# Optimization experiments

Measured on AMD Instinct MI355X. Metric: run time of the kernel, lower is better.

The kernel has to match this reference:

```python
import jax, jax.numpy as jnp
import numpy as np

B, T, D, DS, EXP = 1, 2048, 512, 32, 2
EPS = 1e-6


def setup_inputs() -> dict:
    key = jax.random.key(0)
    ks = jax.random.split(key, 16)
    g = lambda k, shape, s: jax.random.normal(k, shape, jnp.float32) * s
    x = jax.random.normal(ks[0], (B, T, D), jnp.float32)
    inv = D ** -0.5
    return {
        "x": x,
        "norm_w": jnp.ones((D,), jnp.float32),
        "W_in": g(ks[1], (D, 2 * D), inv),
        "conv_w": g(ks[2], (D, 1, 4), 0.5),          # depthwise, torch layout (O, I/groups, K)
        "conv_b": g(ks[3], (D,), 0.1),
        "W_dt": g(ks[4], (D, D), 0.01 * inv),
        "b_dt": jnp.full((D,), -8.0, jnp.float32) + g(ks[5], (D,), 0.1),  # Mamba-style small-dt init
        "W_B": g(ks[6], (D, DS), inv),
        "W_C": g(ks[7], (D, DS), inv),
        "W_out": g(ks[8], (D, D), inv),
        "log_A": jnp.log(jnp.linspace(1.0, 16.0, D)).astype(jnp.float32),
        "D_param": jnp.ones((D,), jnp.float32),
        "W_ffn1": g(ks[9], (D, EXP * D), inv),
        "W_ffn2": g(ks[10], (EXP * D, D), (EXP * D) ** -0.5),
        "W_merge": g(ks[11], (2 * D, D), (2 * D) ** -0.5),
    }


def _ssm_scan(xs, dt, Bm, Cm, A):
    # cumsum-based parallel scan, exactly as ParallelSSMScan.forward
    log_a = jnp.clip(dt * A[None, None, :], -20.0, 20.0)      # [B,T,D]
    cum = jnp.cumsum(log_a, axis=1)                            # [B,T,D]
    dtx = dt * xs                                              # [B,T,D]
    inp = dtx[..., None] * Bm[:, :, None, :]                   # [B,T,D,ds]
    scaled = jnp.exp(-cum)[..., None] * inp                    # [B,T,D,ds]
    prefix = jnp.cumsum(scaled, axis=1)                        # [B,T,D,ds]
    h_all = jnp.exp(cum)[..., None] * prefix                   # [B,T,D,ds]
    return jnp.einsum('btds,bts->btd', h_all, Cm)


def _forward(x, norm_w, W_in, conv_w, conv_b, W_dt, b_dt, W_B, W_C, W_out,
             log_A, D_param, W_ffn1, W_ffn2, W_merge):
    r = x
    rms = jnp.sqrt(jnp.mean(x * x, axis=-1, keepdims=True) + EPS)
    xn = x / rms * norm_w
    xz = xn @ W_in
    xs, z = jnp.split(xz, 2, axis=-1)
    # causal depthwise conv (padding=3 then [:T] == left-pad 3, valid)
    xt = jnp.transpose(xs, (0, 2, 1))                          # [B,D,T]
    c = jax.lax.conv_general_dilated(
        xt, conv_w, window_strides=(1,), padding=[(3, 0)],
        feature_group_count=D, dimension_numbers=('NCH', 'OIH', 'NCH'))
    c = c + conv_b[None, :, None]
    xs = jax.nn.silu(jnp.transpose(c, (0, 2, 1)))              # [B,T,D]
    dt = jax.nn.softplus(xs @ W_dt + b_dt)
    Bm = xs @ W_B
    Cm = xs @ W_C
    A = -jnp.exp(log_A)
    y = _ssm_scan(xs, dt, Bm, Cm, A)
    y_ssm = (y + xs * D_param) * jax.nn.silu(z)
    y_ssm = y_ssm @ W_out
    y_ffn = jax.nn.gelu(xn @ W_ffn1, approximate=False) @ W_ffn2
    y = jnp.concatenate([y_ssm, y_ffn], axis=-1) @ W_merge
    # dropout in eval mode -> identity
    return r + y


def reference(x, norm_w, W_in, conv_w, conv_b, W_dt, b_dt, W_B, W_C, W_out,
              log_A, D_param, W_ffn1, W_ffn2, W_merge):
    return _forward(x, norm_w, W_in, conv_w, conv_b, W_dt, b_dt, W_B, W_C,
                    W_out, log_A, D_param, W_ffn1, W_ffn2, W_merge)
```

## Files before the change

kernel.cpp:

```cpp
#include <hip/hip_runtime.h>
#include <math.h>

#define T_LEN 2048
#define D_DIM 512
#define NCHUNK 64
#define CLEN 32

typedef __bf16 bf16x8 __attribute__((ext_vector_type(8)));
typedef float f32x4 __attribute__((ext_vector_type(4)));

typedef const __attribute__((address_space(1))) void gvoid;
typedef __attribute__((address_space(3))) void lvoid;

__device__ __forceinline__ void async16(const void* g, void* l) {
  __builtin_amdgcn_global_load_lds((gvoid*)g, (lvoid*)l, 16, 0, 0);
}

__device__ __forceinline__ float silu_f(float x) { return x / (1.f + __expf(-x)); }
__device__ __forceinline__ float softplus_f(float x) {
  return fmaxf(x, 0.f) + log1pf(__expf(-fabsf(x)));
}
__device__ __forceinline__ float gelu_f(float x) {
  return 0.5f * x * (1.f + erff(x * 0.70710678118654752440f));
}
__device__ __forceinline__ unsigned short f2bf(float f) {
  union { float f; unsigned u; } v; v.f = f;
  unsigned r = v.u + 0x7FFF + ((v.u >> 16) & 1);
  return (unsigned short)(r >> 16);
}

__global__ __launch_bounds__(256) void rmsnorm_kernel(
    const float* __restrict__ x, const float* __restrict__ w,
    unsigned short* __restrict__ xn) {
  const int t = blockIdx.x;
  const float2 v = reinterpret_cast<const float2*>(x + (size_t)t * D_DIM)[threadIdx.x];
  float ss = v.x * v.x + v.y * v.y;
#pragma unroll
  for (int m = 1; m < 64; m <<= 1) ss += __shfl_xor(ss, m);
  __shared__ float wsum[4];
  if ((threadIdx.x & 63) == 0) wsum[threadIdx.x >> 6] = ss;
  __syncthreads();
  const float tot = wsum[0] + wsum[1] + wsum[2] + wsum[3];
  const float scale = rsqrtf(tot * (1.f / D_DIM) + 1e-6f);
  const float2 wv = reinterpret_cast<const float2*>(w)[threadIdx.x];
  ushort2 o;
  o.x = f2bf(v.x * scale * wv.x);
  o.y = f2bf(v.y * scale * wv.y);
  reinterpret_cast<ushort2*>(xn + (size_t)t * D_DIM)[threadIdx.x] = o;
}

struct TransJobs {
  const float* src[8];
  unsigned short* dst[8];
  int K[8];
  int N[8];
  int tr[8];
  int b0[9];
};

__global__ __launch_bounds__(256) void prep_weights_kernel(TransJobs J) {
  __shared__ float tile[32][33];
  const int b = blockIdx.x;
  int ji = 0;
#pragma unroll
  for (int i = 1; i < 8; ++i) ji += (b >= J.b0[i]) ? 1 : 0;
  const float* __restrict__ src = J.src[ji];
  unsigned short* __restrict__ dst = J.dst[ji];
  const int K = J.K[ji], N = J.N[ji];
  const int rel = b - J.b0[ji];
  const int nbx = N >> 5;
  const int bx = rel % nbx, by = rel / nbx;
  const int k0 = by * 32, n0 = bx * 32;
  const int i = threadIdx.x & 31;
  const int r = threadIdx.x >> 5;
  if (J.tr[ji]) {
#pragma unroll
    for (int p = 0; p < 4; ++p) {
      const int kk = r + p * 8;
      tile[kk][i] = src[(size_t)(k0 + kk) * N + n0 + i];
    }
    __syncthreads();
#pragma unroll
    for (int p = 0; p < 4; ++p) {
      const int nn = r + p * 8;
      dst[(size_t)(n0 + nn) * K + k0 + i] = f2bf(tile[i][nn]);
    }
  } else {
#pragma unroll
    for (int p = 0; p < 4; ++p) {
      const int kk = r + p * 8;
      dst[(size_t)(k0 + kk) * N + n0 + i] = f2bf(src[(size_t)(k0 + kk) * N + n0 + i]);
    }
  }
}

__device__ __forceinline__ void gemm64_core(
    const unsigned short* __restrict__ Abf, const unsigned short* __restrict__ Btbf,
    int nt, int lda8, int ldb8, int brow, int bcol,
    bf16x8* __restrict__ As, bf16x8* __restrict__ Bs, f32x4 acc[2][2]) {
  const int tid = threadIdx.x;
  const int lane = tid & 63;
  const int w = tid >> 6;
  const int wrow = (w >> 1) * 32;
  const int wcol = (w & 1) * 32;
  const bf16x8* __restrict__ A8 = reinterpret_cast<const bf16x8*>(Abf);
  const bf16x8* __restrict__ B8 = reinterpret_cast<const bf16x8*>(Btbf);

  const int lr = lane >> 3;
  const int ls = (lane & 7) ^ lr;
  bf16x8* ldsA0 = &As[(w * 8) * 8];
  bf16x8* ldsA1 = &As[(32 + w * 8) * 8];
  bf16x8* ldsB0 = &Bs[(w * 8) * 8];
  bf16x8* ldsB1 = &Bs[(32 + w * 8) * 8];
  const size_t a0 = (size_t)(brow + w * 8 + lr) * lda8 + ls;
  const size_t a1 = (size_t)(brow + 32 + w * 8 + lr) * lda8 + ls;
  const size_t b0 = (size_t)(bcol + w * 8 + lr) * ldb8 + ls;
  const size_t b1 = (size_t)(bcol + 32 + w * 8 + lr) * ldb8 + ls;

  for (int t = 0; t < nt; ++t) {
    const int kb = t * 8;
    async16(A8 + a0 + kb, ldsA0);
    async16(A8 + a1 + kb, ldsA1);
    async16(B8 + b0 + kb, ldsB0);
    async16(B8 + b1 + kb, ldsB1);
    __syncthreads();
#pragma unroll
    for (int kk = 0; kk < 2; ++kk) {
      const int slot = kk * 4 + (lane >> 4);
      bf16x8 af[2], bf_[2];
#pragma unroll
      for (int m = 0; m < 2; ++m) {
        const int r = wrow + m * 16 + (lane & 15);
        af[m] = As[r * 8 + (slot ^ (r & 7))];
      }
#pragma unroll
      for (int n = 0; n < 2; ++n) {
        const int r = wcol + n * 16 + (lane & 15);
        bf_[n] = Bs[r * 8 + (slot ^ (r & 7))];
      }
#pragma unroll
      for (int m = 0; m < 2; ++m)
#pragma unroll
        for (int n = 0; n < 2; ++n)
          acc[m][n] = __builtin_amdgcn_mfma_f32_16x16x32_bf16(af[m], bf_[n], acc[m][n], 0, 0, 0);
    }
    __syncthreads();
  }
}

__global__ __launch_bounds__(256) void gemm64_in(
    const unsigned short* __restrict__ Abf, const unsigned short* __restrict__ Btbf,
    float* __restrict__ xz, unsigned short* __restrict__ comb) {
  __shared__ bf16x8 As[512];
  __shared__ bf16x8 Bs[512];
  f32x4 acc[2][2];
#pragma unroll
  for (int m = 0; m < 2; ++m)
#pragma unroll
    for (int n = 0; n < 2; ++n) acc[m][n] = {0.f, 0.f, 0.f, 0.f};
  const int brow = blockIdx.y * 64;
  const int bcol = blockIdx.x * 64;
  gemm64_core(Abf, Btbf, 8, 64, 64, brow, bcol, As, Bs, acc);

  const int lane = threadIdx.x & 63;
  const int w = threadIdx.x >> 6;
  const int wrow = (w >> 1) * 32;
  const int wcol = (w & 1) * 32;
#pragma unroll
  for (int m = 0; m < 2; ++m) {
#pragma unroll
    for (int n = 0; n < 2; ++n) {
      const int col = bcol + wcol + n * 16 + (lane & 15);
#pragma unroll
      for (int j = 0; j < 4; ++j) {
        const int row = brow + wrow + m * 16 + (lane >> 4) * 4 + j;
        const float v = acc[m][n][j];
        if (col < 1024) {
          xz[(size_t)row * 1024 + col] = v;
        } else {
          comb[(size_t)row * 1536 + 512 + (col - 1024)] = f2bf(gelu_f(v));
        }
      }
    }
  }
}

__global__ __launch_bounds__(256) void gemm64_dtbc(
    const unsigned short* __restrict__ Abf, const unsigned short* __restrict__ Btbf,
    float* __restrict__ dt, float* __restrict__ Bm, float* __restrict__ Cm,
    const float* __restrict__ bias) {
  __shared__ bf16x8 As[512];
  __shared__ bf16x8 Bs[512];
  f32x4 acc[2][2];
#pragma unroll
  for (int m = 0; m < 2; ++m)
#pragma unroll
    for (int n = 0; n < 2; ++n) acc[m][n] = {0.f, 0.f, 0.f, 0.f};
  const int brow = blockIdx.y * 64;
  const int bcol = blockIdx.x * 64;
  gemm64_core(Abf, Btbf, 8, 64, 64, brow, bcol, As, Bs, acc);

  const int lane = threadIdx.x & 63;
  const int w = threadIdx.x >> 6;
  const int wrow = (w >> 1) * 32;
  const int wcol = (w & 1) * 32;
#pragma unroll
  for (int m = 0; m < 2; ++m) {
#pragma unroll
    for (int n = 0; n < 2; ++n) {
      const int col = bcol + wcol + n * 16 + (lane & 15);
#pragma unroll
      for (int j = 0; j < 4; ++j) {
        const int row = brow + wrow + m * 16 + (lane >> 4) * 4 + j;
        const float v = acc[m][n][j];
        if (col < 512) {
          dt[(size_t)row * 512 + col] = softplus_f(v + bias[col]);
        } else {
          const int s = col - 512;
          float* p = (s < 32) ? Bm : Cm;
          p[(size_t)row * 32 + (s & 31)] = v;
        }
      }
    }
  }
}

__global__ __launch_bounds__(256) void combine_kernel(
    const unsigned short* __restrict__ WmT, const unsigned short* __restrict__ WoutBF,
    const unsigned short* __restrict__ Wf2BF, unsigned short* __restrict__ WcombT) {
  const int z = blockIdx.z;
  if (z == 0 && blockIdx.x >= 8) return;
  __shared__ bf16x8 As[512];
  __shared__ bf16x8 Bs[512];
  const unsigned short* A = z ? (WmT + 512) : WmT;
  const unsigned short* Bt = z ? Wf2BF : WoutBF;
  const int coff = z ? 512 : 0;
  f32x4 acc[2][2];
#pragma unroll
  for (int m = 0; m < 2; ++m)
#pragma unroll
    for (int n = 0; n < 2; ++n) acc[m][n] = {0.f, 0.f, 0.f, 0.f};
  const int brow = blockIdx.y * 64;
  const int bcol = blockIdx.x * 64;
  gemm64_core(A, Bt, 8, 128, 64, brow, bcol, As, Bs, acc);

  const int lane = threadIdx.x & 63;
  const int w = threadIdx.x >> 6;
  const int wrow = (w >> 1) * 32;
  const int wcol = (w & 1) * 32;
#pragma unroll
  for (int m = 0; m < 2; ++m) {
#pragma unroll
    for (int n = 0; n < 2; ++n) {
      const int col = bcol + wcol + n * 16 + (lane & 15);
#pragma unroll
      for (int j = 0; j < 4; ++j) {
        const int row = brow + wrow + m * 16 + (lane >> 4) * 4 + j;
        WcombT[(size_t)row * 1536 + coff + col] = f2bf(acc[m][n][j]);
      }
    }
  }
}

__global__ __launch_bounds__(256) void gemm64_merge(
    const unsigned short* __restrict__ Abf, const unsigned short* __restrict__ Btbf,
    float* __restrict__ out, const float* __restrict__ resid) {
  __shared__ bf16x8 As[512];
  __shared__ bf16x8 Bs[512];
  f32x4 acc[2][2];
#pragma unroll
  for (int m = 0; m < 2; ++m)
#pragma unroll
    for (int n = 0; n < 2; ++n) acc[m][n] = {0.f, 0.f, 0.f, 0.f};
  const int brow = blockIdx.y * 64;
  const int bcol = blockIdx.x * 64;
  gemm64_core(Abf, Btbf, 24, 192, 192, brow, bcol, As, Bs, acc);

  const int lane = threadIdx.x & 63;
  const int w = threadIdx.x >> 6;
  const int wrow = (w >> 1) * 32;
  const int wcol = (w & 1) * 32;
#pragma unroll
  for (int m = 0; m < 2; ++m) {
#pragma unroll
    for (int n = 0; n < 2; ++n) {
      const int col = bcol + wcol + n * 16 + (lane & 15);
#pragma unroll
      for (int j = 0; j < 4; ++j) {
        const int row = brow + wrow + m * 16 + (lane >> 4) * 4 + j;
        out[(size_t)row * 512 + col] = resid[(size_t)row * 512 + col] + acc[m][n][j];
      }
    }
  }
}

__global__ __launch_bounds__(256) void conv_silu_kernel(
    const float* __restrict__ xz, const float* __restrict__ cw,
    const float* __restrict__ cb, float* __restrict__ xs,
    unsigned short* __restrict__ xs_bf) {
  const int idx = blockIdx.x * 256 + threadIdx.x;
  const int t = idx >> 9;
  const int d = idx & 511;
  const float4 w = reinterpret_cast<const float4*>(cw)[d];
  float acc = cb[d];
  const float wk[4] = {w.x, w.y, w.z, w.w};
#pragma unroll
  for (int k = 0; k < 4; ++k) {
    const int tt = t - 3 + k;
    if (tt >= 0) acc = fmaf(xz[(size_t)tt * 1024 + d], wk[k], acc);
  }
  const float s = silu_f(acc);
  xs[idx] = s;
  xs_bf[idx] = f2bf(s);
}

__global__ __launch_bounds__(256) void prep_gram_kernel(
    const float* __restrict__ dt, const float* __restrict__ xs,
    const float* __restrict__ Bm, const float* __restrict__ Cm,
    const float* __restrict__ log_A,
    unsigned short* __restrict__ U_T, float* __restrict__ E,
    float* __restrict__ V, float* __restrict__ Pc,
    unsigned short* __restrict__ Gm) {
  __shared__ float4 Bls4[CLEN * 8];
  __shared__ float Bls[32][33], Cls[32][33];

  if (blockIdx.x < 128) {
    const int c = blockIdx.x >> 1;
    const int d = (blockIdx.x & 1) * 256 + threadIdx.x;
    Bls4[threadIdx.x] = reinterpret_cast<const float4*>(Bm + c * CLEN * 32)[threadIdx.x];
    __syncthreads();

    const float A = -__expf(log_A[d]);
    float cum = 0.f;
    float e = 1.f;
    float vacc[32];
#pragma unroll
    for (int s = 0; s < 32; ++s) vacc[s] = 0.f;
    unsigned pk[16];
#pragma unroll
    for (int t = 0; t < CLEN; ++t) {
      const int tg = c * CLEN + t;
      const float dtv = dt[(size_t)tg * D_DIM + d];
      const float xv  = xs[(size_t)tg * D_DIM + d];
      const float la = fminf(fmaxf(dtv * A, -20.f), 20.f);
      cum += la;
      e = __expf(cum);
      E[(size_t)tg * D_DIM + d] = e;
      const float u = __expf(-cum) * dtv * xv;
      const unsigned short ub = f2bf(u);
      if ((t & 1) == 0) pk[t >> 1] = (unsigned)ub;
      else              pk[t >> 1] |= ((unsigned)ub) << 16;
#pragma unroll
      for (int s4 = 0; s4 < 8; ++s4) {
        const float4 b = Bls4[t * 8 + s4];
        vacc[s4 * 4 + 0] = fmaf(u, b.x, vacc[s4 * 4 + 0]);
        vacc[s4 * 4 + 1] = fmaf(u, b.y, vacc[s4 * 4 + 1]);
        vacc[s4 * 4 + 2] = fmaf(u, b.z, vacc[s4 * 4 + 2]);
        vacc[s4 * 4 + 3] = fmaf(u, b.w, vacc[s4 * 4 + 3]);
      }
    }
    {
      uint4* dst = reinterpret_cast<uint4*>(U_T + (size_t)d * T_LEN + c * CLEN);
      dst[0] = make_uint4(pk[0], pk[1], pk[2], pk[3]);
      dst[1] = make_uint4(pk[4], pk[5], pk[6], pk[7]);
      dst[2] = make_uint4(pk[8], pk[9], pk[10], pk[11]);
      dst[3] = make_uint4(pk[12], pk[13], pk[14], pk[15]);
    }
    {
      float4* dst = reinterpret_cast<float4*>(V + ((size_t)c * D_DIM + d) * 32);
#pragma unroll
      for (int s4 = 0; s4 < 8; ++s4)
        dst[s4] = make_float4(vacc[s4 * 4], vacc[s4 * 4 + 1], vacc[s4 * 4 + 2], vacc[s4 * 4 + 3]);
    }
    Pc[c * D_DIM + d] = e;
  } else {
    const int c = blockIdx.x - 128;
    {
      const int t = threadIdx.x >> 3;
      const int s4 = threadIdx.x & 7;
      const float4 b = reinterpret_cast<const float4*>(Bm + (c * CLEN + t) * 32)[s4];
      const float4 cc = reinterpret_cast<const float4*>(Cm + (c * CLEN + t) * 32)[s4];
      Bls[t][s4 * 4 + 0] = b.x;  Bls[t][s4 * 4 + 1] = b.y;
      Bls[t][s4 * 4 + 2] = b.z;  Bls[t][s4 * 4 + 3] = b.w;
      Cls[t][s4 * 4 + 0] = cc.x; Cls[t][s4 * 4 + 1] = cc.y;
      Cls[t][s4 * 4 + 2] = cc.z; Cls[t][s4 * 4 + 3] = cc.w;
    }
    __syncthreads();
    const int t = threadIdx.x >> 3;
    const int tp0 = (threadIdx.x & 7) * 4;
    float g[4];
#pragma unroll
    for (int q = 0; q < 4; ++q) {
      const int tp = tp0 + q;
      float acc = 0.f;
      if (tp <= t) {
#pragma unroll
        for (int s = 0; s < 32; ++s) acc = fmaf(Cls[t][s], Bls[tp][s], acc);
      }
      g[q] = acc;
    }
    ushort4 o;
    o.x = f2bf(g[0]); o.y = f2bf(g[1]); o.z = f2bf(g[2]); o.w = f2bf(g[3]);
    reinterpret_cast<ushort4*>(Gm + c * 1024)[threadIdx.x] = o;
  }
}

__global__ __launch_bounds__(256) void state_scan_kernel(
    const float* __restrict__ V, const float* __restrict__ Pc,
    float* __restrict__ Hin) {
  const int gt = blockIdx.x * 256 + threadIdx.x;
  const int d = gt >> 5;
  float h = 0.f;
  for (int c = 0; c < NCHUNK; ++c) {
    Hin[c * 16384 + gt] = h;
    h = Pc[c * D_DIM + d] * (h + V[c * 16384 + gt]);
  }
}

__global__ __launch_bounds__(256) void ssm_out_kernel(
    const unsigned short* __restrict__ Gm, const unsigned short* __restrict__ U_T,
    const float* __restrict__ Hin, const float* __restrict__ Cm,
    const float* __restrict__ E, const float* __restrict__ xs,
    const float* __restrict__ Dp, const float* __restrict__ xz,
    unsigned short* __restrict__ comb) {
  const int c = blockIdx.x;
  const int dt0 = blockIdx.y * 64;
  __shared__ bf16x8 Als[32 * 8];
  __shared__ bf16x8 Bls[64 * 8];
  const int tid = threadIdx.x;

  if (tid < 128) {
    const int t = tid >> 2, q = tid & 3;
    Als[t * 8 + (q ^ (t & 7))] =
        *reinterpret_cast<const bf16x8*>(Gm + c * 1024 + t * 32 + q * 8);
  } else {
    const int i = tid - 128;
    const int t = i >> 2, q = i & 3;
    const float* cp = Cm + (c * CLEN + t) * 32 + q * 8;
    const float4 c0 = *reinterpret_cast<const float4*>(cp);
    const float4 c1 = *reinterpret_cast<const float4*>(cp + 4);
    union { bf16x8 v; unsigned short u[8]; } wv;
    wv.u[0] = f2bf(c0.x); wv.u[1] = f2bf(c0.y); wv.u[2] = f2bf(c0.z); wv.u[3] = f2bf(c0.w);
    wv.u[4] = f2bf(c1.x); wv.u[5] = f2bf(c1.y); wv.u[6] = f2bf(c1.z); wv.u[7] = f2bf(c1.w);
    Als[t * 8 + ((4 + q) ^ (t & 7))] = wv.v;
  }
  {
    const int dd = tid >> 2, q = tid & 3;
    Bls[dd * 8 + (q ^ (dd & 7))] = *reinterpret_cast<const bf16x8*>(
        U_T + (size_t)(dt0 + dd) * T_LEN + c * CLEN + q * 8);
    const float* hp = Hin + ((size_t)c * D_DIM + dt0 + dd) * 32 + q * 8;
    const float4 h0 = *reinterpret_cast<const float4*>(hp);
    const float4 h1 = *reinterpret_cast<const float4*>(hp + 4);
    union { bf16x8 v; unsigned short u[8]; } wv;
    wv.u[0] = f2bf(h0.x); wv.u[1] = f2bf(h0.y); wv.u[2] = f2bf(h0.z); wv.u[3] = f2bf(h0.w);
    wv.u[4] = f2bf(h1.x); wv.u[5] = f2bf(h1.y); wv.u[6] = f2bf(h1.z); wv.u[7] = f2bf(h1.w);
    Bls[dd * 8 + ((4 + q) ^ (dd & 7))] = wv.v;
  }
  __syncthreads();

  const int lane = tid & 63;
  const int w = tid >> 6;
  const int wcol = w * 16;
  f32x4 acc[2];
  acc[0] = {0.f, 0.f, 0.f, 0.f};
  acc[1] = {0.f, 0.f, 0.f, 0.f};
#pragma unroll
  for (int kk = 0; kk < 2; ++kk) {
    const int slot = kk * 4 + (lane >> 4);
    const int rb = wcol + (lane & 15);
    const bf16x8 bfrag = Bls[rb * 8 + (slot ^ (rb & 7))];
#pragma unroll
    for (int m = 0; m < 2; ++m) {
      const int r = m * 16 + (lane & 15);
      const bf16x8 afrag = Als[r * 8 + (slot ^ (r & 7))];
      acc[m] = __builtin_amdgcn_mfma_f32_16x16x32_bf16(afrag, bfrag, acc[m], 0, 0, 0);
    }
  }
  const int dg = dt0 + wcol + (lane & 15);
  const float dpv = Dp[dg];
#pragma unroll
  for (int m = 0; m < 2; ++m) {
#pragma unroll
    for (int j = 0; j < 4; ++j) {
      const int tg = c * CLEN + m * 16 + (lane >> 4) * 4 + j;
      const float y = E[(size_t)tg * D_DIM + dg] * acc[m][j];
      const float xv = xs[(size_t)tg * D_DIM + dg];
      const float zv = xz[(size_t)tg * 1024 + 512 + dg];
      comb[(size_t)tg * 1536 + dg] = f2bf(fmaf(xv, dpv, y) * silu_f(zv));
    }
  }
}

extern "C" void kernel_launch(void* const* d_in, const int* in_sizes, int n_in,
                              void* d_out, int out_size, void* d_ws, size_t ws_size,
                              hipStream_t stream) {
  const float* x      = (const float*)d_in[0];
  const float* norm_w = (const float*)d_in[1];
  const float* W_in   = (const float*)d_in[2];
  const float* conv_w = (const float*)d_in[3];
  const float* conv_b = (const float*)d_in[4];
  const float* W_dt   = (const float*)d_in[5];
  const float* b_dt   = (const float*)d_in[6];
  const float* W_B    = (const float*)d_in[7];
  const float* W_C    = (const float*)d_in[8];
  const float* W_out  = (const float*)d_in[9];
  const float* log_A  = (const float*)d_in[10];
  const float* D_par  = (const float*)d_in[11];
  const float* W_ffn1 = (const float*)d_in[12];
  const float* W_ffn2 = (const float*)d_in[13];
  const float* W_mrg  = (const float*)d_in[14];
  float* out = (float*)d_out;

  const size_t M1 = 1u << 20;
  char* ws = (char*)d_ws;
  size_t off = 0;
  auto alloc_f = [&](size_t n) { float* p = (float*)(ws + off); off += n * 4; return p; };
  auto alloc_h = [&](size_t n) { unsigned short* p = (unsigned short*)(ws + off); off += n * 2; return p; };

  float* xz  = alloc_f(2 * M1);
  float* xs  = alloc_f(M1);
  float* dt  = alloc_f(M1);
  float* E   = alloc_f(M1);
  float* V   = alloc_f(M1);
  float* Hin = alloc_f(M1);
  float* Bm  = alloc_f(1 << 16);
  float* Cm  = alloc_f(1 << 16);
  float* Pc  = alloc_f(NCHUNK * D_DIM);
  unsigned short* U_T    = alloc_h(M1);
  unsigned short* Gm     = alloc_h(NCHUNK * 1024);
  unsigned short* xn_bf  = alloc_h(M1);
  unsigned short* xs_bf  = alloc_h(M1);
  unsigned short* comb   = alloc_h(2048 * 1536);
  unsigned short* WinF1T = alloc_h(2048 * 512);
  unsigned short* WdtBCT = alloc_h(576 * 512);
  unsigned short* WmT    = alloc_h(512 * 1024);
  unsigned short* WoutBF = alloc_h(512 * 512);
  unsigned short* Wf2BF  = alloc_h(1024 * 512);
  unsigned short* WcombT = alloc_h(512 * 1536);

  TransJobs J;
  J.src[0] = W_in;   J.dst[0] = WinF1T;              J.K[0] = 512;  J.N[0] = 1024; J.tr[0] = 1;
  J.src[1] = W_ffn1; J.dst[1] = WinF1T + 1024 * 512; J.K[1] = 512;  J.N[1] = 1024; J.tr[1] = 1;
  J.src[2] = W_dt;   J.dst[2] = WdtBCT;              J.K[2] = 512;  J.N[2] = 512;  J.tr[2] = 1;
  J.src[3] = W_B;    J.dst[3] = WdtBCT + 512 * 512;  J.K[3] = 512;  J.N[3] = 32;   J.tr[3] = 1;
  J.src[4] = W_C;    J.dst[4] = WdtBCT + 544 * 512;  J.K[4] = 512;  J.N[4] = 32;   J.tr[4] = 1;
  J.src[5] = W_mrg;  J.dst[5] = WmT;                 J.K[5] = 1024; J.N[5] = 512;  J.tr[5] = 1;
  J.src[6] = W_out;  J.dst[6] = WoutBF;              J.K[6] = 512;  J.N[6] = 512;  J.tr[6] = 0;
  J.src[7] = W_ffn2; J.dst[7] = Wf2BF;               J.K[7] = 1024; J.N[7] = 512;  J.tr[7] = 0;
  int bacc = 0;
  for (int i = 0; i < 8; ++i) {
    J.b0[i] = bacc;
    bacc += (J.N[i] >> 5) * (J.K[i] >> 5);
  }
  J.b0[8] = bacc;
  prep_weights_kernel<<<bacc, 256, 0, stream>>>(J);

  combine_kernel<<<dim3(16, 8, 2), 256, 0, stream>>>(WmT, WoutBF, Wf2BF, WcombT);

  rmsnorm_kernel<<<T_LEN, 256, 0, stream>>>(x, norm_w, xn_bf);
  gemm64_in<<<dim3(32, 32), 256, 0, stream>>>(xn_bf, WinF1T, xz, comb);
  conv_silu_kernel<<<4096, 256, 0, stream>>>(xz, conv_w, conv_b, xs, xs_bf);
  gemm64_dtbc<<<dim3(9, 32), 256, 0, stream>>>(xs_bf, WdtBCT, dt, Bm, Cm, b_dt);
  prep_gram_kernel<<<192, 256, 0, stream>>>(dt, xs, Bm, Cm, log_A, U_T, E, V, Pc, Gm);
  state_scan_kernel<<<64, 256, 0, stream>>>(V, Pc, Hin);
  ssm_out_kernel<<<dim3(NCHUNK, 8), 256, 0, stream>>>(Gm, U_T, Hin, Cm, E, xs, D_par, xz, comb);
  gemm64_merge<<<dim3(8, 32), 256, 0, stream>>>(comb, WcombT, out, x);
}
```

Before: 90.63 us.

## Fuse launches and double-buffer LDS tiles in GEMM core

Merges the weight-prep and RMSNorm kernels into one launch, and merges the input GEMM with the weight-combine GEMMs into one grid partitioned by block index. This removes two kernel launches and the serialization gaps between them. The shared GEMM core now double-buffers its LDS tiles, issuing the async loads for the next K-step before computing the current one, so it needs one barrier per iteration instead of two. LDS use per block doubles, which may reduce occupancy.

```diff
diff --git a/kernel.cpp b/kernel.cpp
--- a/kernel.cpp
+++ b/kernel.cpp
@@ -27,26 +27,6 @@
   union { float f; unsigned u; } v; v.f = f;
   unsigned r = v.u + 0x7FFF + ((v.u >> 16) & 1);
   return (unsigned short)(r >> 16);
-}
-
-__global__ __launch_bounds__(256) void rmsnorm_kernel(
-    const float* __restrict__ x, const float* __restrict__ w,
-    unsigned short* __restrict__ xn) {
-  const int t = blockIdx.x;
-  const float2 v = reinterpret_cast<const float2*>(x + (size_t)t * D_DIM)[threadIdx.x];
-  float ss = v.x * v.x + v.y * v.y;
-#pragma unroll
-  for (int m = 1; m < 64; m <<= 1) ss += __shfl_xor(ss, m);
-  __shared__ float wsum[4];
-  if ((threadIdx.x & 63) == 0) wsum[threadIdx.x >> 6] = ss;
-  __syncthreads();
-  const float tot = wsum[0] + wsum[1] + wsum[2] + wsum[3];
-  const float scale = rsqrtf(tot * (1.f / D_DIM) + 1e-6f);
-  const float2 wv = reinterpret_cast<const float2*>(w)[threadIdx.x];
-  ushort2 o;
-  o.x = f2bf(v.x * scale * wv.x);
-  o.y = f2bf(v.y * scale * wv.y);
-  reinterpret_cast<ushort2*>(xn + (size_t)t * D_DIM)[threadIdx.x] = o;
 }
 
 struct TransJobs {
@@ -58,9 +38,29 @@
   int b0[9];
 };
 
-__global__ __launch_bounds__(256) void prep_weights_kernel(TransJobs J) {
+__global__ __launch_bounds__(256) void prep_rms_kernel(
+    TransJobs J, const float* __restrict__ x, const float* __restrict__ nw,
+    unsigned short* __restrict__ xn) {
+  const int b = blockIdx.x;
+  if (b >= J.b0[8]) {
+    const int t = b - J.b0[8];
+    const float2 v = reinterpret_cast<const float2*>(x + (size_t)t * D_DIM)[threadIdx.x];
+    float ss = v.x * v.x + v.y * v.y;
+#pragma unroll
+    for (int m = 1; m < 64; m <<= 1) ss += __shfl_xor(ss, m);
+    __shared__ float wsum[4];
+    if ((threadIdx.x & 63) == 0) wsum[threadIdx.x >> 6] = ss;
+    __syncthreads();
+    const float tot = wsum[0] + wsum[1] + wsum[2] + wsum[3];
+    const float scale = rsqrtf(tot * (1.f / D_DIM) + 1e-6f);
+    const float2 wv = reinterpret_cast<const float2*>(nw)[threadIdx.x];
+    ushort2 o;
+    o.x = f2bf(v.x * scale * wv.x);
+    o.y = f2bf(v.y * scale * wv.y);
+    reinterpret_cast<ushort2*>(xn + (size_t)t * D_DIM)[threadIdx.x] = o;
+    return;
+  }
   __shared__ float tile[32][33];
-  const int b = blockIdx.x;
   int ji = 0;
 #pragma unroll
   for (int i = 1; i < 8; ++i) ji += (b >= J.b0[i]) ? 1 : 0;
@@ -108,22 +108,30 @@
 
   const int lr = lane >> 3;
   const int ls = (lane & 7) ^ lr;
-  bf16x8* ldsA0 = &As[(w * 8) * 8];
-  bf16x8* ldsA1 = &As[(32 + w * 8) * 8];
-  bf16x8* ldsB0 = &Bs[(w * 8) * 8];
-  bf16x8* ldsB1 = &Bs[(32 + w * 8) * 8];
+  const int wb = w * 64;
   const size_t a0 = (size_t)(brow + w * 8 + lr) * lda8 + ls;
   const size_t a1 = (size_t)(brow + 32 + w * 8 + lr) * lda8 + ls;
   const size_t b0 = (size_t)(bcol + w * 8 + lr) * ldb8 + ls;
   const size_t b1 = (size_t)(bcol + 32 + w * 8 + lr) * ldb8 + ls;
 
+  async16(A8 + a0, As + wb);
+  async16(A8 + a1, As + 256 + wb);
+  async16(B8 + b0, Bs + wb);
+  async16(B8 + b1, Bs + 256 + wb);
+  __syncthreads();
+
+  int cur = 0;
   for (int t = 0; t < nt; ++t) {
-    const int kb = t * 8;
-    async16(A8 + a0 + kb, ldsA0);
-    async16(A8 + a1 + kb, ldsA1);
-    async16(B8 + b0 + kb, ldsB0);
-    async16(B8 + b1 + kb, ldsB1);
-    __syncthreads();
+    if (t + 1 < nt) {
+      const int kb = (t + 1) * 8;
+      const int nx = (cur ^ 1) * 512;
+      async16(A8 + a0 + kb, As + nx + wb);
+      async16(A8 + a1 + kb, As + nx + 256 + wb);
+      async16(B8 + b0 + kb, Bs + nx + wb);
+      async16(B8 + b1 + kb, Bs + nx + 256 + wb);
+    }
+    const bf16x8* __restrict__ Ac = As + cur * 512;
+    const bf16x8* __restrict__ Bc = Bs + cur * 512;
 #pragma unroll
     for (int kk = 0; kk < 2; ++kk) {
       const int slot = kk * 4 + (lane >> 4);
@@ -131,12 +139,12 @@
 #pragma unroll
       for (int m = 0; m < 2; ++m) {
         const int r = wrow + m * 16 + (lane & 15);
-        af[m] = As[r * 8 + (slot ^ (r & 7))];
+        af[m] = Ac[r * 8 + (slot ^ (r & 7))];
       }
 #pragma unroll
       for (int n = 0; n < 2; ++n) {
         const int r = wcol + n * 16 + (lane & 15);
-        bf_[n] = Bs[r * 8 + (slot ^ (r & 7))];
+        bf_[n] = Bc[r * 8 + (slot ^ (r & 7))];
       }
 #pragma unroll
       for (int m = 0; m < 2; ++m)
@@ -145,40 +153,81 @@
           acc[m][n] = __builtin_amdgcn_mfma_f32_16x16x32_bf16(af[m], bf_[n], acc[m][n], 0, 0, 0);
     }
     __syncthreads();
-  }
-}
-
-__global__ __launch_bounds__(256) void gemm64_in(
-    const unsigned short* __restrict__ Abf, const unsigned short* __restrict__ Btbf,
-    float* __restrict__ xz, unsigned short* __restrict__ comb) {
-  __shared__ bf16x8 As[512];
-  __shared__ bf16x8 Bs[512];
+    cur ^= 1;
+  }
+}
+
+__global__ __launch_bounds__(256) void gemm_in_combine(
+    const unsigned short* __restrict__ xn_bf, const unsigned short* __restrict__ WinF1T,
+    float* __restrict__ xz, unsigned short* __restrict__ comb,
+    const unsigned short* __restrict__ WmT, const unsigned short* __restrict__ WoutBF,
+    const unsigned short* __restrict__ Wf2BF, unsigned short* __restrict__ WcombT) {
+  __shared__ bf16x8 As[1024];
+  __shared__ bf16x8 Bs[1024];
   f32x4 acc[2][2];
 #pragma unroll
   for (int m = 0; m < 2; ++m)
 #pragma unroll
     for (int n = 0; n < 2; ++n) acc[m][n] = {0.f, 0.f, 0.f, 0.f};
-  const int brow = blockIdx.y * 64;
-  const int bcol = blockIdx.x * 64;
-  gemm64_core(Abf, Btbf, 8, 64, 64, brow, bcol, As, Bs, acc);
-
+
+  const int b = blockIdx.x;
   const int lane = threadIdx.x & 63;
   const int w = threadIdx.x >> 6;
   const int wrow = (w >> 1) * 32;
   const int wcol = (w & 1) * 32;
-#pragma unroll
-  for (int m = 0; m < 2; ++m) {
-#pragma unroll
-    for (int n = 0; n < 2; ++n) {
-      const int col = bcol + wcol + n * 16 + (lane & 15);
-#pragma unroll
-      for (int j = 0; j < 4; ++j) {
-        const int row = brow + wrow + m * 16 + (lane >> 4) * 4 + j;
-        const float v = acc[m][n][j];
-        if (col < 1024) {
-          xz[(size_t)row * 1024 + col] = v;
-        } else {
-          comb[(size_t)row * 1536 + 512 + (col - 1024)] = f2bf(gelu_f(v));
+
+  if (b < 1024) {
+    const int brow = (b >> 5) * 64;
+    const int bcol = (b & 31) * 64;
+    gemm64_core(xn_bf, WinF1T, 8, 64, 64, brow, bcol, As, Bs, acc);
+#pragma unroll
+    for (int m = 0; m < 2; ++m) {
+#pragma unroll
+      for (int n = 0; n < 2; ++n) {
+        const int col = bcol + wcol + n * 16 + (lane & 15);
+#pragma unroll
+        for (int j = 0; j < 4; ++j) {
+          const int row = brow + wrow + m * 16 + (lane >> 4) * 4 + j;
+          const float v = acc[m][n][j];
+          if (col < 1024) {
+            xz[(size_t)row * 1024 + col] = v;
+          } else {
+            comb[(size_t)row * 1536 + 512 + (col - 1024)] = f2bf(gelu_f(v));
+          }
+        }
+      }
+    }
+  } else if (b < 1088) {
+    const int rel = b - 1024;
+    const int brow = (rel >> 3) * 64;
+    const int bcol = (rel & 7) * 64;
+    gemm64_core(WmT, WoutBF, 8, 128, 64, brow, bcol, As, Bs, acc);
+#pragma unroll
+    for (int m = 0; m < 2; ++m) {
+#pragma unroll
+      for (int n = 0; n < 2; ++n) {
+        const int col = bcol + wcol + n * 16 + (lane & 15);
+#pragma unroll
+        for (int j = 0; j < 4; ++j) {
+          const int row = brow + wrow + m * 16 + (lane >> 4) * 4 + j;
+          WcombT[(size_t)row * 1536 + col] = f2bf(acc[m][n][j]);
+        }
+      }
+    }
+  } else {
+    const int rel = b - 1088;
+    const int brow = (rel >> 4) * 64;
+    const int bcol = (rel & 15) * 64;
+    gemm64_core(WmT + 512, Wf2BF, 8, 128, 64, brow, bcol, As, Bs, acc);
+#pragma unroll
+    for (int m = 0; m < 2; ++m) {
+#pragma unroll
+      for (int n = 0; n < 2; ++n) {
+        const int col = bcol + wcol + n * 16 + (lane & 15);
+#pragma unroll
+        for (int j = 0; j < 4; ++j) {
+          const int row = brow + wrow + m * 16 + (lane >> 4) * 4 + j;
+          WcombT[(size_t)row * 1536 + 512 + col] = f2bf(acc[m][n][j]);
         }
       }
     }
@@ -189,8 +238,8 @@
     const unsigned short* __restrict__ Abf, const unsigned short* __restrict__ Btbf,
     float* __restrict__ dt, float* __restrict__ Bm, float* __restrict__ Cm,
     const float* __restrict__ bias) {
-  __shared__ bf16x8 As[512];
-  __shared__ bf16x8 Bs[512];
+  __shared__ bf16x8 As[1024];
+  __shared__ bf16x8 Bs[1024];
   f32x4 acc[2][2];
 #pragma unroll
   for (int m = 0; m < 2; ++m)
@@ -225,48 +274,11 @@
   }
 }
 
-__global__ __launch_bounds__(256) void combine_kernel(
-    const unsigned short* __restrict__ WmT, const unsigned short* __restrict__ WoutBF,
-    const unsigned short* __restrict__ Wf2BF, unsigned short* __restrict__ WcombT) {
-  const int z = blockIdx.z;
-  if (z == 0 && blockIdx.x >= 8) return;
-  __shared__ bf16x8 As[512];
-  __shared__ bf16x8 Bs[512];
-  const unsigned short* A = z ? (WmT + 512) : WmT;
-  const unsigned short* Bt = z ? Wf2BF : WoutBF;
-  const int coff = z ? 512 : 0;
-  f32x4 acc[2][2];
-#pragma unroll
-  for (int m = 0; m < 2; ++m)
-#pragma unroll
-    for (int n = 0; n < 2; ++n) acc[m][n] = {0.f, 0.f, 0.f, 0.f};
-  const int brow = blockIdx.y * 64;
-  const int bcol = blockIdx.x * 64;
-  gemm64_core(A, Bt, 8, 128, 64, brow, bcol, As, Bs, acc);
-
-  const int lane = threadIdx.x & 63;
-  const int w = threadIdx.x >> 6;
-  const int wrow = (w >> 1) * 32;
-  const int wcol = (w & 1) * 32;
-#pragma unroll
-  for (int m = 0; m < 2; ++m) {
-#pragma unroll
-    for (int n = 0; n < 2; ++n) {
-      const int col = bcol + wcol + n * 16 + (lane & 15);
-#pragma unroll
-      for (int j = 0; j < 4; ++j) {
-        const int row = brow + wrow + m * 16 + (lane >> 4) * 4 + j;
-        WcombT[(size_t)row * 1536 + coff + col] = f2bf(acc[m][n][j]);
-      }
-    }
-  }
-}
-
 __global__ __launch_bounds__(256) void gemm64_merge(
     const unsigned short* __restrict__ Abf, const unsigned short* __restrict__ Btbf,
     float* __restrict__ out, const float* __restrict__ resid) {
-  __shared__ bf16x8 As[512];
-  __shared__ bf16x8 Bs[512];
+  __shared__ bf16x8 As[1024];
+  __shared__ bf16x8 Bs[1024];
   f32x4 acc[2][2];
 #pragma unroll
   for (int m = 0; m < 2; ++m)
@@ -553,12 +565,10 @@
     bacc += (J.N[i] >> 5) * (J.K[i] >> 5);
   }
   J.b0[8] = bacc;
-  prep_weights_kernel<<<bacc, 256, 0, stream>>>(J);
-
-  combine_kernel<<<dim3(16, 8, 2), 256, 0, stream>>>(WmT, WoutBF, Wf2BF, WcombT);
-
-  rmsnorm_kernel<<<T_LEN, 256, 0, stream>>>(x, norm_w, xn_bf);
-  gemm64_in<<<dim3(32, 32), 256, 0, stream>>>(xn_bf, WinF1T, xz, comb);
+  prep_rms_kernel<<<bacc + T_LEN, 256, 0, stream>>>(J, x, norm_w, xn_bf);
+
+  gemm_in_combine<<<1216, 256, 0, stream>>>(
+      xn_bf, WinF1T, xz, comb, WmT, WoutBF, Wf2BF, WcombT);
   conv_silu_kernel<<<4096, 256, 0, stream>>>(xz, conv_w, conv_b, xs, xs_bf);
   gemm64_dtbc<<<dim3(9, 32), 256, 0, stream>>>(xs_bf, WdtBCT, dt, Bm, Cm, b_dt);
   prep_gram_kernel<<<192, 256, 0, stream>>>(dt, xs, Bm, Cm, log_A, U_T, E, V, Pc, Gm);
```

Measured after the change: 89.56 us. Within noise of the previous version (-1.2%).
